# Optimization experiments

Hardware: AMD Instinct MI355X
Metric: run time of the kernel (lower is better)

Reference implementation:

```python
import jax, jax.numpy as jnp
import numpy as np

B, N, D_V, D_MODEL, D_FF, N_HEADS = 32, 64, 6, 128, 512, 8


def _ln(x, g, b):
    m = x.mean(-1, keepdims=True)
    v = ((x - m) ** 2).mean(-1, keepdims=True)
    return (x - m) / jnp.sqrt(v + 1e-5) * g + b


def _mha(q_in, k_in, v_in, mask, Wq, Wk, Wv, Wo):
    # mask: (b, Lq, Lk) bool, True = attend
    b, Lq, D = q_in.shape
    H, dh = N_HEADS, D_MODEL // N_HEADS
    q = (q_in @ Wq).reshape(b, Lq, H, dh)
    k = (k_in @ Wk).reshape(b, k_in.shape[1], H, dh)
    v = (v_in @ Wv).reshape(b, v_in.shape[1], H, dh)
    s = jnp.einsum('bqhd,bkhd->bhqk', q, k) / (dh ** 0.5)
    s = jnp.where(mask[:, None, :, :], s, -1e9)
    o = jnp.einsum('bhqk,bkhd->bqhd', jax.nn.softmax(s, axis=-1), v).reshape(b, Lq, D)
    return o @ Wo


def setup_inputs() -> dict:
    key = jax.random.key(0)
    ks = jax.random.split(key, 40)
    def p(i, shape, scale=0.05):
        return jax.random.normal(ks[i], shape, dtype=jnp.float32) * scale
    nm = jax.random.randint(ks[1], (B, N, N), 0, 2, dtype=jnp.int32)
    nm = nm.at[:, jnp.arange(N), jnp.arange(N)].set(1)  # self always a neighbor
    inp = {
        'agent_infos': jax.random.normal(ks[0], (B, N, N, D_V), dtype=jnp.float32),
        'neighbor_masks': nm,
        'padding_mask': jnp.ones((B, N), dtype=jnp.int32),
        'is_from_my_env': jnp.ones((B,), dtype=jnp.int32),
        # src_embed
        'W_emb': p(2, (D_V, D_MODEL)), 'b_emb': jnp.zeros((D_MODEL,), jnp.float32),
        # encoder layer (self-attn + FFN, post-LN)
        'Wq': p(3, (D_MODEL, D_MODEL)), 'Wk': p(4, (D_MODEL, D_MODEL)),
        'Wv': p(5, (D_MODEL, D_MODEL)), 'Wo': p(6, (D_MODEL, D_MODEL)),
        'ln1_g': jnp.ones((D_MODEL,), jnp.float32), 'ln1_b': jnp.zeros((D_MODEL,), jnp.float32),
        'W1': p(7, (D_MODEL, D_FF)), 'b1': jnp.zeros((D_FF,), jnp.float32),
        'W2': p(8, (D_FF, D_MODEL)), 'b2': jnp.zeros((D_MODEL,), jnp.float32),
        'ln2_g': jnp.ones((D_MODEL,), jnp.float32), 'ln2_b': jnp.zeros((D_MODEL,), jnp.float32),
        # decoder layer (cross-attn + FFN, post-LN)
        'Uq': p(9, (D_MODEL, D_MODEL)), 'Uk': p(10, (D_MODEL, D_MODEL)),
        'Uv': p(11, (D_MODEL, D_MODEL)), 'Uo': p(12, (D_MODEL, D_MODEL)),
        'ln3_g': jnp.ones((D_MODEL,), jnp.float32), 'ln3_b': jnp.zeros((D_MODEL,), jnp.float32),
        'W3': p(13, (D_MODEL, D_FF)), 'b3': jnp.zeros((D_FF,), jnp.float32),
        'W4': p(14, (D_FF, D_MODEL)), 'b4': jnp.zeros((D_MODEL,), jnp.float32),
        'ln4_g': jnp.ones((D_MODEL,), jnp.float32), 'ln4_b': jnp.zeros((D_MODEL,), jnp.float32),
        # generator (single-head query/key scorer)
        'Wg_q': p(15, (D_MODEL, D_MODEL)), 'Wg_k': p(16, (D_MODEL, D_MODEL)),
    }
    return inp


def reference(agent_infos, neighbor_masks, padding_mask, is_from_my_env,
              W_emb, b_emb, Wq, Wk, Wv, Wo, ln1_g, ln1_b, W1, b1, W2, b2, ln2_g, ln2_b,
              Uq, Uk, Uv, Uo, ln3_g, ln3_b, W3, b3, W4, b4, ln4_g, ln4_b, Wg_q, Wg_k):
    # Fold the per-agent python loop of the original into the batch dim: BN = B * N.
    src = agent_infos.reshape(B * N, N, D_V)
    neigh = neighbor_masks.reshape(B * N, N) != 0           # True = neighbor (attendable)
    x = src @ W_emb + b_emb                                 # (BN, N, D)
    src_mask = neigh[:, :, None] & neigh[:, None, :]        # (BN, N, N)
    x = _ln(x + _mha(x, x, x, src_mask, Wq, Wk, Wv, Wo), ln1_g, ln1_b)
    x = _ln(x + (jax.nn.relu(x @ W1 + b1) @ W2 + b2), ln2_g, ln2_b)
    # context vector -- faithful to the original get_context_vector (which sums rows
    # where pad_tokens==True, i.e. NON-neighbors, and divides by the neighbor count)
    pad = (~neigh)[:, :, None].astype(x.dtype)
    cnt = neigh.sum(axis=1).reshape(-1, 1, 1).astype(x.dtype)
    h_c = (x * pad).sum(axis=1, keepdims=True) / cnt        # (BN, 1, D)
    stm = neigh[:, None, :]                                 # src_tgt_mask (BN, 1, N)
    y = _ln(h_c + _mha(h_c, x, x, stm, Uq, Uk, Uv, Uo), ln3_g, ln3_b)
    y = _ln(y + (jax.nn.relu(y @ W3 + b3) @ W4 + b4), ln4_g, ln4_b)
    logits = jnp.einsum('bqd,bkd->bqk', y @ Wg_q, x @ Wg_k) / (D_MODEL ** 0.5)
    probs = jnp.where(stm, jax.nn.sigmoid(logits), 0.0)[:, 0, :]   # (BN, N)
    att_scores = probs.reshape(B, N, N)
    num_agents = padding_mask.sum(axis=1).astype(x.dtype).reshape(B, 1, 1)
    avg_h_c_N = h_c.reshape(B, N, D_MODEL).sum(axis=1, keepdims=True) / num_agents
    return att_scores, avg_h_c_N
```

## Files before the change

### kernel.cpp

```cpp
#include <hip/hip_runtime.h>
#include <hip/hip_bf16.h>
#include <math.h>

#define ITEMS 2048
#define SEQ   64
#define DM    128
#define DFF   512
#define ATT_OFF 131072

typedef unsigned short u16;
typedef __attribute__((ext_vector_type(4))) unsigned short ushort4v;
typedef __attribute__((ext_vector_type(8))) short short8v;
typedef __attribute__((ext_vector_type(4))) float float4v;

#define MFMA16(a,b,c) __builtin_amdgcn_mfma_f32_16x16x32_bf16(a,b,c,0,0,0)

#define XST 136
#define VST 72
#define PST 76

#define XS_B   0
#define QS_B   17408
#define KS_B   34816
#define VT_B   52224
#define PL_B   70656
#define ZB_B   80384
#define PF_B   80400
#define CNT_B  80656
#define NA_B   80660
#define NB_B   80664
#define ARENA_SZ 80672

#define HC_B   (KS_B+0)
#define QV_B   (KS_B+512)
#define OV_B   (KS_B+1024)
#define YV_B   (KS_B+1536)
#define Y2_B   (KS_B+2048)
#define GW_B   (KS_B+2560)
#define WALL_B (VT_B+0)
#define SALL_B (VT_B+4096)
#define PALL_B (VT_B+6144)
#define TALL_B (VT_B+8192)
#define FF_B   (VT_B+12288)
#define W4P_B  (VT_B+14336)

#define WQ_O   0
#define WK_O   16384
#define WV_O   32768
#define WO_O   49152
#define UK_O   65536
#define UV_O   81920
#define W1_O   98304
#define W2_O   163840
#define UQ_O   229376
#define UO_O   245760
#define WGQ_O  262144
#define WGK_O  278528
#define W3_O   294912
#define W4_O   360448
#define WS_TOT 425984

__device__ __forceinline__ u16 f2b(float f){
  union { float f; unsigned u; } v; v.f = f;
  unsigned r = (v.u + 0x7fffu + ((v.u >> 16) & 1u)) >> 16;
  return (u16)r;
}
__device__ __forceinline__ float b2f(u16 h){
  union { unsigned u; float f; } v; v.u = ((unsigned)h) << 16;
  return v.f;
}
__device__ __forceinline__ float wsum(float v){
  #pragma unroll
  for (int off = 1; off < 64; off <<= 1) v += __shfl_xor(v, off);
  return v;
}
__device__ __forceinline__ void ln_vec(float* v, const float* g, const float* b, int lane){
  float v0 = v[lane], v1 = v[lane+64];
  float m  = wsum(v0+v1) * (1.f/128.f);
  float d0 = v0-m, d1 = v1-m;
  float var = wsum(d0*d0+d1*d1) * (1.f/128.f);
  float inv = rsqrtf(var + 1e-5f);
  v[lane]    = d0*inv*g[lane]    + b[lane];
  v[lane+64] = d1*inv*g[lane+64] + b[lane+64];
}
__device__ __forceinline__ float dot128(const u16* __restrict__ wrow, const float* __restrict__ x){
  const short8v* wr = (const short8v*)wrow;
  float a = 0.f;
  #pragma unroll
  for (int c8 = 0; c8 < 16; c8++){
    short8v v = wr[c8];
    #pragma unroll
    for (int q = 0; q < 8; q++) a += b2f((u16)v[q]) * x[c8*8+q];
  }
  return a;
}

__global__ void prep_all(const float* __restrict__ Wq, const float* __restrict__ Wk,
                         const float* __restrict__ Wv, const float* __restrict__ Wo,
                         const float* __restrict__ Uk, const float* __restrict__ Uv,
                         const float* __restrict__ W1, const float* __restrict__ W2,
                         const float* __restrict__ Uq, const float* __restrict__ Uo,
                         const float* __restrict__ Wgq, const float* __restrict__ Wgk,
                         const float* __restrict__ W3, const float* __restrict__ W4,
                         u16* __restrict__ wts){
  int idx = blockIdx.x*256 + threadIdx.x;
  if (idx >= WS_TOT) return;
  float v;
  if (idx < 98304){
    int wsel = idx >> 14, r = idx & 16383;
    const float* tab[6] = {Wq,Wk,Wv,Wo,Uk,Uv};
    int o = r >> 7, i = r & 127;
    v = tab[wsel][i*128 + o];
  } else if (idx < W2_O){
    int r = idx - W1_O; int o = r >> 7, i = r & 127;
    v = W1[i*512 + o];
  } else if (idx < UQ_O){
    int r = idx - W2_O; int o = r >> 9, i = r & 511;
    v = W2[i*128 + o];
  } else if (idx < UO_O){
    int r = idx - UQ_O; int o = r >> 7, i = r & 127;
    v = Uq[i*128 + o];
  } else if (idx < WGQ_O){
    int r = idx - UO_O; int o = r >> 7, i = r & 127;
    v = Uo[i*128 + o];
  } else if (idx < WGK_O){
    int r = idx - WGQ_O; int o = r >> 7, i = r & 127;
    v = Wgq[i*128 + o];
  } else if (idx < W3_O){
    v = Wgk[idx - WGK_O];
  } else if (idx < W4_O){
    int r = idx - W3_O; int j = r >> 7, e = r & 127;
    v = W3[e*512 + j];
  } else {
    int r = idx - W4_O; int o = r >> 9, j = r & 511;
    v = W4[j*128 + o];
  }
  wts[idx] = f2b(v);
}

__global__ void init_avg(float* __restrict__ out){
  out[ATT_OFF + blockIdx.x*256 + threadIdx.x] = 0.f;
}

__global__ __launch_bounds__(256, 2) void vicsek_fused(
    const float* __restrict__ agent_infos,
    const int*   __restrict__ nmask,
    const int*   __restrict__ pmask,
    const u16*   __restrict__ wts,
    const float* __restrict__ W_emb, const float* __restrict__ b_emb,
    const float* __restrict__ ln1g,  const float* __restrict__ ln1b,
    const float* __restrict__ b1,    const float* __restrict__ b2,
    const float* __restrict__ ln2g,  const float* __restrict__ ln2b,
    const float* __restrict__ ln3g,  const float* __restrict__ ln3b,
    const float* __restrict__ b3,    const float* __restrict__ b4,
    const float* __restrict__ ln4g,  const float* __restrict__ ln4b,
    float* __restrict__ out)
{
  __shared__ __align__(16) char arena[ARENA_SZ];
  u16* Xs = (u16*)(arena + XS_B);
  u16* Qs = (u16*)(arena + QS_B);
  u16* Ks = (u16*)(arena + KS_B);
  u16* VT = (u16*)(arena + VT_B);
  u16* Pl = (u16*)(arena + PL_B);
  u16* zb = (u16*)(arena + ZB_B);
  float* padf  = (float*)(arena + PF_B);
  float* cnt_s = (float*)(arena + CNT_B);
  float* na_s  = (float*)(arena + NA_B);
  unsigned long long* nb_s = (unsigned long long*)(arena + NB_B);

  const int item = blockIdx.x;
  const int tid  = threadIdx.x;
  const int lane = tid & 63;
  const int w    = tid >> 6;
  const int row0 = w*16;
  const int arow = lane & 15;
  const int akg  = lane >> 4;

  const u16* WqT = wts + WQ_O;  const u16* WkT = wts + WK_O;
  const u16* WvT = wts + WV_O;  const u16* WoT = wts + WO_O;
  const u16* UkT = wts + UK_O;  const u16* UvT = wts + UV_O;
  const u16* W1T = wts + W1_O;  const u16* W2T = wts + W2_O;
  const u16* UqT = wts + UQ_O;  const u16* UoT = wts + UO_O;
  const u16* WgqT = wts + WGQ_O; const u16* WgkB = wts + WGK_O;
  const u16* W3T = wts + W3_O;  const u16* W4T = wts + W4_O;

  if (w == 0){
    int m = nmask[item*SEQ + lane];
    padf[lane] = m ? 0.f : 1.f;
    float c = wsum(m ? 1.f : 0.f);
    unsigned long long bb = __ballot(m != 0);
    if (lane == 0){ cnt_s[0] = c; nb_s[0] = bb; }
  }
  if (w == 1){
    float na = wsum((float)pmask[(item>>6)*SEQ + lane]);
    if (lane == 0) na_s[0] = na;
  }
  if (tid < 8) zb[tid] = 0;

  const float* src = agent_infos + (size_t)item*SEQ*6;
  for (int e = tid; e < SEQ*DM; e += 256){
    int r = e >> 7, c = e & 127;
    float a = b_emb[c];
    #pragma unroll
    for (int k = 0; k < 6; k++) a += src[r*6+k]*W_emb[k*DM+c];
    Xs[r*XST + c] = f2b(a);
  }
  __syncthreads();

  const unsigned long long nbits = nb_s[0];

  short8v aX[4];
  #pragma unroll
  for (int k = 0; k < 4; k++) aX[k] = *(const short8v*)(Xs + (row0+arow)*XST + k*32 + akg*8);

  for (int t = 0; t < 8; t++){
    const u16* wq = WqT + (t*16+arow)*128 + akg*8;
    const u16* wk = WkT + (t*16+arow)*128 + akg*8;
    const u16* wv = WvT + (t*16+arow)*128 + akg*8;
    float4v cq = {0,0,0,0}, ck = {0,0,0,0}, cv = {0,0,0,0};
    #pragma unroll
    for (int k = 0; k < 4; k++){
      cq = MFMA16(aX[k], *(const short8v*)(wq + k*32), cq);
      ck = MFMA16(aX[k], *(const short8v*)(wk + k*32), ck);
      cv = MFMA16(*(const short8v*)(wv + k*32), aX[k], cv);
    }
    #pragma unroll
    for (int i = 0; i < 4; i++){
      Qs[(row0+akg*4+i)*XST + t*16+arow] = f2b(cq[i]);
      Ks[(row0+akg*4+i)*XST + t*16+arow] = f2b(ck[i]);
      VT[(t*16+akg*4+i)*VST + row0+arow] = f2b(cv[i]);
    }
  }
  float4v accW[8];
  #pragma unroll
  for (int t = 0; t < 8; t++)
    #pragma unroll
    for (int i = 0; i < 4; i++)
      accW[t][i] = b2f(Xs[(row0+akg*4+i)*XST + t*16 + arow]);
  __syncthreads();

  for (int h = 0; h < 8; h++){
    const u16* qp = (akg < 2) ? (Qs + (row0+arow)*XST + h*16 + akg*8) : zb;
    short8v bq = *(const short8v*)qp;
    float4v st[4];
    #pragma unroll
    for (int kb = 0; kb < 4; kb++){
      const u16* kp = (akg < 2) ? (Ks + (kb*16+arow)*XST + h*16 + akg*8) : zb;
      float4v z = {0,0,0,0};
      st[kb] = MFMA16(*(const short8v*)kp, bq, z);
    }
    bool qok = (nbits >> (row0+arow)) & 1ull;
    float pr[16]; float mx = -3.0e38f;
    #pragma unroll
    for (int kb = 0; kb < 4; kb++)
      #pragma unroll
      for (int i = 0; i < 4; i++){
        int key = kb*16 + akg*4 + i;
        float s = st[kb][i]*0.25f;
        if (!qok || !((nbits>>key)&1ull)) s = -1.0e9f;
        pr[kb*4+i] = s; mx = fmaxf(mx, s);
      }
    mx = fmaxf(mx, __shfl_xor(mx,16)); mx = fmaxf(mx, __shfl_xor(mx,32));
    float sum = 0.f;
    #pragma unroll
    for (int z = 0; z < 16; z++){ pr[z] = __expf(pr[z]-mx); sum += pr[z]; }
    sum += __shfl_xor(sum,16); sum += __shfl_xor(sum,32);
    float inv = 1.f/sum;
    #pragma unroll
    for (int kb = 0; kb < 4; kb++)
      #pragma unroll
      for (int i = 0; i < 4; i++)
        Pl[(kb*16+akg*4+i)*PST + row0+arow] = f2b(pr[kb*4+i]*inv);
    float4v ot = {0,0,0,0};
    #pragma unroll
    for (int c2 = 0; c2 < 2; c2++){
      short8v av = *(const short8v*)(VT + (h*16+arow)*VST + c2*32 + akg*8);
      short8v bp;
      #pragma unroll
      for (int j = 0; j < 8; j++) bp[j] = (short)Pl[(c2*32+akg*8+j)*PST + row0+arow];
      ot = MFMA16(av, bp, ot);
    }
    ushort4v ov4;
    #pragma unroll
    for (int i = 0; i < 4; i++) ov4[i] = f2b(ot[i]);
    *(ushort4v*)(Xs + (row0+arow)*XST + h*16 + akg*4) = ov4;
  }

  {
    short8v aO[4];
    #pragma unroll
    for (int k = 0; k < 4; k++) aO[k] = *(const short8v*)(Xs + (row0+arow)*XST + k*32 + akg*8);
    #pragma unroll
    for (int k = 0; k < 4; k++)
      #pragma unroll
      for (int t = 0; t < 8; t++)
        accW[t] = MFMA16(aO[k], *(const short8v*)(WoT + (t*16+arow)*128 + k*32 + akg*8), accW[t]);
    float g8[8], bb8[8];
    #pragma unroll
    for (int t = 0; t < 8; t++){ g8[t] = ln1g[t*16+arow]; bb8[t] = ln1b[t*16+arow]; }
    #pragma unroll
    for (int i = 0; i < 4; i++){
      float sm = 0.f;
      #pragma unroll
      for (int t = 0; t < 8; t++) sm += accW[t][i];
      sm += __shfl_xor(sm,1); sm += __shfl_xor(sm,2); sm += __shfl_xor(sm,4); sm += __shfl_xor(sm,8);
      float mean = sm*(1.f/128.f);
      float vs = 0.f;
      #pragma unroll
      for (int t = 0; t < 8; t++){ float d = accW[t][i]-mean; vs += d*d; }
      vs += __shfl_xor(vs,1); vs += __shfl_xor(vs,2); vs += __shfl_xor(vs,4); vs += __shfl_xor(vs,8);
      float inv = rsqrtf(vs*(1.f/128.f) + 1e-5f);
      #pragma unroll
      for (int t = 0; t < 8; t++)
        Xs[(row0+akg*4+i)*XST + t*16 + arow] = f2b((accW[t][i]-mean)*inv*g8[t] + bb8[t]);
    }
  }
  #pragma unroll
  for (int k = 0; k < 4; k++) aX[k] = *(const short8v*)(Xs + (row0+arow)*XST + k*32 + akg*8);

  {
    u16* Hb = Qs;
    float4v accY[8];
    #pragma unroll
    for (int t = 0; t < 8; t++){
      float bb = b2[t*16 + arow];
      #pragma unroll
      for (int i = 0; i < 4; i++)
        accY[t][i] = bb + b2f(Xs[(row0+akg*4+i)*XST + t*16 + arow]);
    }
    for (int c = 0; c < 4; c++){
      #pragma unroll
      for (int t = 0; t < 8; t++){
        float bb = b1[c*128 + t*16 + arow];
        float4v acc = {bb,bb,bb,bb};
        #pragma unroll
        for (int k = 0; k < 4; k++)
          acc = MFMA16(aX[k], *(const short8v*)(W1T + (c*128+t*16+arow)*128 + k*32 + akg*8), acc);
        #pragma unroll
        for (int i = 0; i < 4; i++)
          Hb[(row0+akg*4+i)*XST + t*16 + arow] = f2b(fmaxf(acc[i], 0.f));
      }
      #pragma unroll
      for (int k = 0; k < 4; k++){
        short8v aH = *(const short8v*)(Hb + (row0+arow)*XST + k*32 + akg*8);
        #pragma unroll
        for (int t = 0; t < 8; t++)
          accY[t] = MFMA16(aH, *(const short8v*)(W2T + (t*16+arow)*512 + c*128 + k*32 + akg*8), accY[t]);
      }
    }
    float g8[8], bb8[8];
    #pragma unroll
    for (int t = 0; t < 8; t++){ g8[t] = ln2g[t*16+arow]; bb8[t] = ln2b[t*16+arow]; }
    #pragma unroll
    for (int i = 0; i < 4; i++){
      float sm = 0.f;
      #pragma unroll
      for (int t = 0; t < 8; t++) sm += accY[t][i];
      sm += __shfl_xor(sm,1); sm += __shfl_xor(sm,2); sm += __shfl_xor(sm,4); sm += __shfl_xor(sm,8);
      float mean = sm*(1.f/128.f);
      float vs = 0.f;
      #pragma unroll
      for (int t = 0; t < 8; t++){ float d = accY[t][i]-mean; vs += d*d; }
      vs += __shfl_xor(vs,1); vs += __shfl_xor(vs,2); vs += __shfl_xor(vs,4); vs += __shfl_xor(vs,8);
      float inv = rsqrtf(vs*(1.f/128.f) + 1e-5f);
      #pragma unroll
      for (int t = 0; t < 8; t++)
        Xs[(row0+akg*4+i)*XST + t*16 + arow] = f2b((accY[t][i]-mean)*inv*g8[t] + bb8[t]);
    }
  }
  __syncthreads();

  float* hc   = (float*)(arena + HC_B);
  float* qv   = (float*)(arena + QV_B);
  float* ov   = (float*)(arena + OV_B);
  float* yv   = (float*)(arena + YV_B);
  float* y2   = (float*)(arena + Y2_B);
  float* gw   = (float*)(arena + GW_B);
  float* wall = (float*)(arena + WALL_B);
  float* sall = (float*)(arena + SALL_B);
  float* pall = (float*)(arena + PALL_B);
  float* tall = (float*)(arena + TALL_B);
  float* ff   = (float*)(arena + FF_B);
  float* w4p  = (float*)(arena + W4P_B);

  if (tid < DM){
    float a = 0.f;
    #pragma unroll 8
    for (int r = 0; r < SEQ; r++) a += b2f(Xs[r*XST + tid]) * padf[r];
    a /= cnt_s[0];
    hc[tid] = a;
    atomicAdd(&out[ATT_OFF + (item>>6)*DM + tid], a/na_s[0]);
  }
  __syncthreads();

  if (tid < DM) qv[tid] = dot128(UqT + tid*128, hc);
  __syncthreads();
  if (tid < DM){
    #pragma unroll
    for (int h = 0; h < 8; h++){
      float a = 0.f;
      #pragma unroll
      for (int d = 0; d < 16; d++) a += b2f(UkT[(h*16+d)*128 + tid]) * qv[h*16+d];
      wall[h*128 + tid] = a;
    }
  }
  __syncthreads();
  for (int idx = tid; idx < 512; idx += 256){
    int h = idx >> 6, j = idx & 63;
    const short8v* xr = (const short8v*)(Xs + j*XST);
    const float* wv_ = wall + h*128;
    float a = 0.f;
    #pragma unroll
    for (int c8 = 0; c8 < 16; c8++){
      short8v v = xr[c8];
      #pragma unroll
      for (int q = 0; q < 8; q++) a += b2f((u16)v[q]) * wv_[c8*8+q];
    }
    sall[idx] = a*0.25f;
  }
  __syncthreads();
  for (int hh = w; hh < 8; hh += 4){
    float s = sall[hh*64 + lane];
    if (!((nbits>>lane)&1ull)) s = -1.0e9f;
    float mxx = s;
    #pragma unroll
    for (int off = 1; off < 64; off <<= 1) mxx = fmaxf(mxx, __shfl_xor(mxx, off));
    float p = __expf(s - mxx);
    float su = wsum(p);
    pall[hh*64 + lane] = p/su;
  }
  __syncthreads();
  {
    int task = tid >> 1, jh = tid & 1;
    int h = task >> 4, c8 = task & 15;
    float acc8[8] = {0,0,0,0,0,0,0,0};
    #pragma unroll 4
    for (int jj = 0; jj < 32; jj++){
      int j = jh*32 + jj;
      short8v v = *(const short8v*)(Xs + j*XST + c8*8);
      float pj = pall[h*64 + j];
      #pragma unroll
      for (int q = 0; q < 8; q++) acc8[q] += pj * b2f((u16)v[q]);
    }
    #pragma unroll
    for (int q = 0; q < 8; q++) acc8[q] += __shfl_xor(acc8[q], 1);
    if (jh == 0){
      #pragma unroll
      for (int q = 0; q < 8; q++) tall[h*128 + c8*8 + q] = acc8[q];
    }
  }
  __syncthreads();
  if (tid < DM) ov[tid] = dot128(UvT + tid*128, tall + (tid>>4)*128);
  __syncthreads();
  if (tid < DM) yv[tid] = hc[tid] + dot128(UoT + tid*128, ov);
  __syncthreads();
  if (w == 0) ln_vec(yv, ln3g, ln3b, lane);
  __syncthreads();

  for (int j = tid; j < DFF; j += 256)
    ff[j] = fmaxf(b3[j] + dot128(W3T + j*128, yv), 0.f);
  __syncthreads();
  {
    int o = tid & 127, half = tid >> 7;
    const short8v* wr = (const short8v*)(W4T + o*512 + half*256);
    const float* fh = ff + half*256;
    float a = 0.f;
    #pragma unroll
    for (int c8 = 0; c8 < 32; c8++){
      short8v v = wr[c8];
      #pragma unroll
      for (int q = 0; q < 8; q++) a += b2f((u16)v[q]) * fh[c8*8+q];
    }
    w4p[tid] = a;
  }
  __syncthreads();
  if (tid < DM) y2[tid] = b4[tid] + yv[tid] + w4p[tid] + w4p[tid+128];
  __syncthreads();
  if (w == 0) ln_vec(y2, ln4g, ln4b, lane);
  __syncthreads();

  if (tid < DM) qv[tid] = dot128(WgqT + tid*128, y2);
  __syncthreads();
  if (tid < DM) gw[tid] = dot128(WgkB + tid*128, qv);
  __syncthreads();
  if (tid < SEQ){
    float a = dot128(Xs + tid*XST, gw) ;
    a *= 0.08838834764831845f;
    out[(size_t)item*SEQ + tid] = ((nbits>>tid)&1ull) ? (1.f/(1.f+__expf(-a))) : 0.f;
  }
}

extern "C" void kernel_launch(void* const* d_in, const int* in_sizes, int n_in,
                              void* d_out, int out_size, void* d_ws, size_t ws_size,
                              hipStream_t stream)
{
  const float* agent_infos = (const float*)d_in[0];
  const int*   nmask       = (const int*)  d_in[1];
  const int*   pmask       = (const int*)  d_in[2];
  const float* W_emb = (const float*)d_in[4];
  const float* b_emb = (const float*)d_in[5];
  const float* Wq    = (const float*)d_in[6];
  const float* Wk    = (const float*)d_in[7];
  const float* Wv    = (const float*)d_in[8];
  const float* Wo    = (const float*)d_in[9];
  const float* ln1g  = (const float*)d_in[10];
  const float* ln1b  = (const float*)d_in[11];
  const float* W1    = (const float*)d_in[12];
  const float* b1    = (const float*)d_in[13];
  const float* W2    = (const float*)d_in[14];
  const float* b2    = (const float*)d_in[15];
  const float* ln2g  = (const float*)d_in[16];
  const float* ln2b  = (const float*)d_in[17];
  const float* Uq    = (const float*)d_in[18];
  const float* Uk    = (const float*)d_in[19];
  const float* Uv    = (const float*)d_in[20];
  const float* Uo    = (const float*)d_in[21];
  const float* ln3g  = (const float*)d_in[22];
  const float* ln3b  = (const float*)d_in[23];
  const float* W3    = (const float*)d_in[24];
  const float* b3    = (const float*)d_in[25];
  const float* W4    = (const float*)d_in[26];
  const float* b4    = (const float*)d_in[27];
  const float* ln4g  = (const float*)d_in[28];
  const float* ln4b  = (const float*)d_in[29];
  const float* Wgq   = (const float*)d_in[30];
  const float* Wgk   = (const float*)d_in[31];

  float* out = (float*)d_out;
  u16*   wts = (u16*)d_ws;

  prep_all<<<(WS_TOT+255)/256, 256, 0, stream>>>(Wq, Wk, Wv, Wo, Uk, Uv, W1, W2,
                                                 Uq, Uo, Wgq, Wgk, W3, W4, wts);
  init_avg<<<16, 256, 0, stream>>>(out);
  vicsek_fused<<<ITEMS, 256, 0, stream>>>(
      agent_infos, nmask, pmask, wts, W_emb, b_emb,
      ln1g, ln1b, b1, b2, ln2g, ln2b, ln3g, ln3b,
      b3, b4, ln4g, ln4b, out);
}
```

Measured before the change: 636.1 us.

## Process each item with a single wavefront and shrink shared memory

The fused kernel drops from 256 threads (4 waves) per item to one 64-lane wave that handles all four row groups. QKV projection now runs per head into small per-head buffers, and the LDS arena shrinks from about 80 KB to about 31 KB. All __syncthreads barriers go away, which should allow many more resident blocks per CU. The decoder cross-attention score and weighted-sum steps now use MFMA instead of scalar loops. In exchange, each wave does four times the work serially and holds a large register footprint (aX for all row groups plus packed residuals), which may cause spills or limit occupancy.

```diff
diff --git a/kernel.cpp b/kernel.cpp
--- a/kernel.cpp
+++ b/kernel.cpp
@@ -9,40 +9,38 @@
 #define ATT_OFF 131072
 
 typedef unsigned short u16;
+typedef unsigned int u32;
 typedef __attribute__((ext_vector_type(4))) unsigned short ushort4v;
 typedef __attribute__((ext_vector_type(8))) short short8v;
 typedef __attribute__((ext_vector_type(4))) float float4v;
 
 #define MFMA16(a,b,c) __builtin_amdgcn_mfma_f32_16x16x32_bf16(a,b,c,0,0,0)
 
-#define XST 136
-#define VST 72
-#define PST 76
+#define XST  136
+#define QST1 24
+#define VST1 72
+#define PST  20
 
 #define XS_B   0
-#define QS_B   17408
-#define KS_B   34816
-#define VT_B   52224
-#define PL_B   70656
-#define ZB_B   80384
-#define PF_B   80400
-#define CNT_B  80656
-#define NA_B   80660
-#define NB_B   80664
-#define ARENA_SZ 80672
-
-#define HC_B   (KS_B+0)
-#define QV_B   (KS_B+512)
-#define OV_B   (KS_B+1024)
-#define YV_B   (KS_B+1536)
-#define Y2_B   (KS_B+2048)
-#define GW_B   (KS_B+2560)
-#define WALL_B (VT_B+0)
-#define SALL_B (VT_B+4096)
-#define PALL_B (VT_B+6144)
-#define TALL_B (VT_B+8192)
-#define FF_B   (VT_B+12288)
-#define W4P_B  (VT_B+14336)
+#define Q1_B   17408
+#define K1_B   20480
+#define V1_B   23552
+#define PL_B   25856
+#define HC_B   28416
+#define QV_B   28928
+#define OV_B   29440
+#define YV_B   29952
+#define Y2_B   30464
+#define GW_B   30976
+#define ZB_B   31488
+#define ARENA_SZ 31504
+
+#define HBF_B   17408
+#define WALLB_B 17408
+#define SALL_B  19456
+#define PALL_B  21504
+#define TALL_B  17408
+#define FF_B    23552
 
 #define WQ_O   0
 #define WK_O   16384
@@ -142,7 +140,7 @@
   out[ATT_OFF + blockIdx.x*256 + threadIdx.x] = 0.f;
 }
 
-__global__ __launch_bounds__(256, 2) void vicsek_fused(
+__global__ __launch_bounds__(64, 2) void vicsek_fused(
     const float* __restrict__ agent_infos,
     const int*   __restrict__ nmask,
     const int*   __restrict__ pmask,
@@ -157,22 +155,15 @@
     float* __restrict__ out)
 {
   __shared__ __align__(16) char arena[ARENA_SZ];
-  u16* Xs = (u16*)(arena + XS_B);
-  u16* Qs = (u16*)(arena + QS_B);
-  u16* Ks = (u16*)(arena + KS_B);
-  u16* VT = (u16*)(arena + VT_B);
-  u16* Pl = (u16*)(arena + PL_B);
-  u16* zb = (u16*)(arena + ZB_B);
-  float* padf  = (float*)(arena + PF_B);
-  float* cnt_s = (float*)(arena + CNT_B);
-  float* na_s  = (float*)(arena + NA_B);
-  unsigned long long* nb_s = (unsigned long long*)(arena + NB_B);
+  u16* Xs  = (u16*)(arena + XS_B);
+  u16* Q1  = (u16*)(arena + Q1_B);
+  u16* K1  = (u16*)(arena + K1_B);
+  u16* V1T = (u16*)(arena + V1_B);
+  u16* Pl  = (u16*)(arena + PL_B);
+  u16* zb  = (u16*)(arena + ZB_B);
 
   const int item = blockIdx.x;
-  const int tid  = threadIdx.x;
-  const int lane = tid & 63;
-  const int w    = tid >> 6;
-  const int row0 = w*16;
+  const int lane = threadIdx.x;
   const int arow = lane & 15;
   const int akg  = lane >> 4;
 
@@ -184,309 +175,351 @@
   const u16* WgqT = wts + WGQ_O; const u16* WgkB = wts + WGK_O;
   const u16* W3T = wts + W3_O;  const u16* W4T = wts + W4_O;
 
-  if (w == 0){
-    int m = nmask[item*SEQ + lane];
-    padf[lane] = m ? 0.f : 1.f;
-    float c = wsum(m ? 1.f : 0.f);
-    unsigned long long bb = __ballot(m != 0);
-    if (lane == 0){ cnt_s[0] = c; nb_s[0] = bb; }
-  }
-  if (w == 1){
-    float na = wsum((float)pmask[(item>>6)*SEQ + lane]);
-    if (lane == 0) na_s[0] = na;
-  }
-  if (tid < 8) zb[tid] = 0;
-
-  const float* src = agent_infos + (size_t)item*SEQ*6;
-  for (int e = tid; e < SEQ*DM; e += 256){
-    int r = e >> 7, c = e & 127;
-    float a = b_emb[c];
-    #pragma unroll
-    for (int k = 0; k < 6; k++) a += src[r*6+k]*W_emb[k*DM+c];
-    Xs[r*XST + c] = f2b(a);
-  }
-  __syncthreads();
-
-  const unsigned long long nbits = nb_s[0];
-
-  short8v aX[4];
-  #pragma unroll
-  for (int k = 0; k < 4; k++) aX[k] = *(const short8v*)(Xs + (row0+arow)*XST + k*32 + akg*8);
-
-  for (int t = 0; t < 8; t++){
-    const u16* wq = WqT + (t*16+arow)*128 + akg*8;
-    const u16* wk = WkT + (t*16+arow)*128 + akg*8;
-    const u16* wv = WvT + (t*16+arow)*128 + akg*8;
-    float4v cq = {0,0,0,0}, ck = {0,0,0,0}, cv = {0,0,0,0};
-    #pragma unroll
-    for (int k = 0; k < 4; k++){
-      cq = MFMA16(aX[k], *(const short8v*)(wq + k*32), cq);
-      ck = MFMA16(aX[k], *(const short8v*)(wk + k*32), ck);
-      cv = MFMA16(*(const short8v*)(wv + k*32), aX[k], cv);
-    }
-    #pragma unroll
-    for (int i = 0; i < 4; i++){
-      Qs[(row0+akg*4+i)*XST + t*16+arow] = f2b(cq[i]);
-      Ks[(row0+akg*4+i)*XST + t*16+arow] = f2b(ck[i]);
-      VT[(t*16+akg*4+i)*VST + row0+arow] = f2b(cv[i]);
-    }
-  }
-  float4v accW[8];
-  #pragma unroll
-  for (int t = 0; t < 8; t++)
-    #pragma unroll
-    for (int i = 0; i < 4; i++)
-      accW[t][i] = b2f(Xs[(row0+akg*4+i)*XST + t*16 + arow]);
-  __syncthreads();
-
+  if (lane < 8) zb[lane] = 0;
+
+  int mm = nmask[item*SEQ + lane];
+  const unsigned long long nbits = __ballot(mm != 0);
+  const float cnt = (float)__popcll(nbits);
+  unsigned long long pb = __ballot(pmask[(item>>6)*SEQ + lane] != 0);
+  const float na = (float)__popcll(pb);
+
+  {
+    const float* src = agent_infos + (size_t)item*SEQ*6;
+    float we0[6], we1[6];
+    #pragma unroll
+    for (int k = 0; k < 6; k++){ we0[k] = W_emb[k*DM+lane]; we1[k] = W_emb[k*DM+lane+64]; }
+    float be0 = b_emb[lane], be1 = b_emb[lane+64];
+    for (int r = 0; r < SEQ; r++){
+      float a0 = be0, a1 = be1;
+      #pragma unroll
+      for (int k = 0; k < 6; k++){ float s = src[r*6+k]; a0 += s*we0[k]; a1 += s*we1[k]; }
+      Xs[r*XST + lane]    = f2b(a0);
+      Xs[r*XST + lane+64] = f2b(a1);
+    }
+  }
+
+  short8v aX[4][4];
+  #pragma unroll
+  for (int rg = 0; rg < 4; rg++)
+    #pragma unroll
+    for (int k = 0; k < 4; k++)
+      aX[rg][k] = *(const short8v*)(Xs + (rg*16+arow)*XST + k*32 + akg*8);
+  u32 resid[4][8][2];
+  #pragma unroll
+  for (int rg = 0; rg < 4; rg++)
+    #pragma unroll
+    for (int t = 0; t < 8; t++){
+      u16 x0 = Xs[(rg*16+akg*4+0)*XST + t*16+arow];
+      u16 x1 = Xs[(rg*16+akg*4+1)*XST + t*16+arow];
+      u16 x2 = Xs[(rg*16+akg*4+2)*XST + t*16+arow];
+      u16 x3 = Xs[(rg*16+akg*4+3)*XST + t*16+arow];
+      resid[rg][t][0] = (u32)x0 | ((u32)x1 << 16);
+      resid[rg][t][1] = (u32)x2 | ((u32)x3 << 16);
+    }
+
+  #pragma unroll 1
   for (int h = 0; h < 8; h++){
-    const u16* qp = (akg < 2) ? (Qs + (row0+arow)*XST + h*16 + akg*8) : zb;
-    short8v bq = *(const short8v*)qp;
-    float4v st[4];
-    #pragma unroll
-    for (int kb = 0; kb < 4; kb++){
-      const u16* kp = (akg < 2) ? (Ks + (kb*16+arow)*XST + h*16 + akg*8) : zb;
-      float4v z = {0,0,0,0};
-      st[kb] = MFMA16(*(const short8v*)kp, bq, z);
-    }
-    bool qok = (nbits >> (row0+arow)) & 1ull;
-    float pr[16]; float mx = -3.0e38f;
-    #pragma unroll
-    for (int kb = 0; kb < 4; kb++)
+    {
+      short8v bw[4];
+      #pragma unroll
+      for (int k = 0; k < 4; k++) bw[k] = *(const short8v*)(WqT + (h*16+arow)*128 + k*32 + akg*8);
+      #pragma unroll
+      for (int rg = 0; rg < 4; rg++){
+        float4v c = {0,0,0,0};
+        #pragma unroll
+        for (int k = 0; k < 4; k++) c = MFMA16(aX[rg][k], bw[k], c);
+        #pragma unroll
+        for (int i = 0; i < 4; i++) Q1[(rg*16+akg*4+i)*QST1 + arow] = f2b(c[i]);
+      }
+      #pragma unroll
+      for (int k = 0; k < 4; k++) bw[k] = *(const short8v*)(WkT + (h*16+arow)*128 + k*32 + akg*8);
+      #pragma unroll
+      for (int rg = 0; rg < 4; rg++){
+        float4v c = {0,0,0,0};
+        #pragma unroll
+        for (int k = 0; k < 4; k++) c = MFMA16(aX[rg][k], bw[k], c);
+        #pragma unroll
+        for (int i = 0; i < 4; i++) K1[(rg*16+akg*4+i)*QST1 + arow] = f2b(c[i]);
+      }
+      #pragma unroll
+      for (int k = 0; k < 4; k++) bw[k] = *(const short8v*)(WvT + (h*16+arow)*128 + k*32 + akg*8);
+      #pragma unroll
+      for (int rg = 0; rg < 4; rg++){
+        float4v c = {0,0,0,0};
+        #pragma unroll
+        for (int k = 0; k < 4; k++) c = MFMA16(bw[k], aX[rg][k], c);
+        #pragma unroll
+        for (int i = 0; i < 4; i++) V1T[(akg*4+i)*VST1 + rg*16+arow] = f2b(c[i]);
+      }
+    }
+    for (int qt = 0; qt < 4; qt++){
+      const u16* qp = (akg < 2) ? (Q1 + (qt*16+arow)*QST1 + akg*8) : zb;
+      short8v bq = *(const short8v*)qp;
+      float4v st[4];
+      #pragma unroll
+      for (int kb = 0; kb < 4; kb++){
+        const u16* kp = (akg < 2) ? (K1 + (kb*16+arow)*QST1 + akg*8) : zb;
+        float4v z = {0,0,0,0};
+        st[kb] = MFMA16(*(const short8v*)kp, bq, z);
+      }
+      bool qok = (nbits >> (qt*16+arow)) & 1ull;
+      float pr[16]; float mx = -3.0e38f;
+      #pragma unroll
+      for (int kb = 0; kb < 4; kb++)
+        #pragma unroll
+        for (int i = 0; i < 4; i++){
+          int key = kb*16 + akg*4 + i;
+          float s = st[kb][i]*0.25f;
+          if (!qok || !((nbits>>key)&1ull)) s = -1.0e9f;
+          pr[kb*4+i] = s; mx = fmaxf(mx, s);
+        }
+      mx = fmaxf(mx, __shfl_xor(mx,16)); mx = fmaxf(mx, __shfl_xor(mx,32));
+      float sum = 0.f;
+      #pragma unroll
+      for (int z2 = 0; z2 < 16; z2++){ pr[z2] = __expf(pr[z2]-mx); sum += pr[z2]; }
+      sum += __shfl_xor(sum,16); sum += __shfl_xor(sum,32);
+      float inv = 1.f/sum;
+      #pragma unroll
+      for (int kb = 0; kb < 4; kb++)
+        #pragma unroll
+        for (int i = 0; i < 4; i++)
+          Pl[(kb*16+akg*4+i)*PST + arow] = f2b(pr[kb*4+i]*inv);
+      float4v ot = {0,0,0,0};
+      #pragma unroll
+      for (int c2 = 0; c2 < 2; c2++){
+        short8v av = *(const short8v*)(V1T + arow*VST1 + c2*32 + akg*8);
+        short8v bp;
+        #pragma unroll
+        for (int j = 0; j < 8; j++) bp[j] = (short)Pl[(c2*32+akg*8+j)*PST + arow];
+        ot = MFMA16(av, bp, ot);
+      }
+      ushort4v ov4;
+      #pragma unroll
+      for (int i = 0; i < 4; i++) ov4[i] = f2b(ot[i]);
+      *(ushort4v*)(Xs + (qt*16+arow)*XST + h*16 + akg*4) = ov4;
+    }
+  }
+
+  {
+    float g8[8], bb8[8];
+    #pragma unroll
+    for (int t = 0; t < 8; t++){ g8[t] = ln1g[t*16+arow]; bb8[t] = ln1b[t*16+arow]; }
+    #pragma unroll
+    for (int rg = 0; rg < 4; rg++){
+      float4v acc[8];
+      #pragma unroll
+      for (int t = 0; t < 8; t++){
+        acc[t][0] = b2f((u16)(resid[rg][t][0] & 0xffff));
+        acc[t][1] = b2f((u16)(resid[rg][t][0] >> 16));
+        acc[t][2] = b2f((u16)(resid[rg][t][1] & 0xffff));
+        acc[t][3] = b2f((u16)(resid[rg][t][1] >> 16));
+      }
+      short8v aO[4];
+      #pragma unroll
+      for (int k = 0; k < 4; k++) aO[k] = *(const short8v*)(Xs + (rg*16+arow)*XST + k*32 + akg*8);
+      #pragma unroll
+      for (int k = 0; k < 4; k++)
+        #pragma unroll
+        for (int t = 0; t < 8; t++)
+          acc[t] = MFMA16(aO[k], *(const short8v*)(WoT + (t*16+arow)*128 + k*32 + akg*8), acc[t]);
       #pragma unroll
       for (int i = 0; i < 4; i++){
-        int key = kb*16 + akg*4 + i;
-        float s = st[kb][i]*0.25f;
-        if (!qok || !((nbits>>key)&1ull)) s = -1.0e9f;
-        pr[kb*4+i] = s; mx = fmaxf(mx, s);
-      }
-    mx = fmaxf(mx, __shfl_xor(mx,16)); mx = fmaxf(mx, __shfl_xor(mx,32));
-    float sum = 0.f;
-    #pragma unroll
-    for (int z = 0; z < 16; z++){ pr[z] = __expf(pr[z]-mx); sum += pr[z]; }
-    sum += __shfl_xor(sum,16); sum += __shfl_xor(sum,32);
-    float inv = 1.f/sum;
-    #pragma unroll
-    for (int kb = 0; kb < 4; kb++)
-      #pragma unroll
-      for (int i = 0; i < 4; i++)
-        Pl[(kb*16+akg*4+i)*PST + row0+arow] = f2b(pr[kb*4+i]*inv);
-    float4v ot = {0,0,0,0};
-    #pragma unroll
-    for (int c2 = 0; c2 < 2; c2++){
-      short8v av = *(const short8v*)(VT + (h*16+arow)*VST + c2*32 + akg*8);
-      short8v bp;
-      #pragma unroll
-      for (int j = 0; j < 8; j++) bp[j] = (short)Pl[(c2*32+akg*8+j)*PST + row0+arow];
-      ot = MFMA16(av, bp, ot);
-    }
-    ushort4v ov4;
-    #pragma unroll
-    for (int i = 0; i < 4; i++) ov4[i] = f2b(ot[i]);
-    *(ushort4v*)(Xs + (row0+arow)*XST + h*16 + akg*4) = ov4;
+        float sm = 0.f;
+        #pragma unroll
+        for (int t = 0; t < 8; t++) sm += acc[t][i];
+        sm += __shfl_xor(sm,1); sm += __shfl_xor(sm,2); sm += __shfl_xor(sm,4); sm += __shfl_xor(sm,8);
+        float mean = sm*(1.f/128.f);
+        float vs = 0.f;
+        #pragma unroll
+        for (int t = 0; t < 8; t++){ float d = acc[t][i]-mean; vs += d*d; }
+        vs += __shfl_xor(vs,1); vs += __shfl_xor(vs,2); vs += __shfl_xor(vs,4); vs += __shfl_xor(vs,8);
+        float inv = rsqrtf(vs*(1.f/128.f) + 1e-5f);
+        #pragma unroll
+        for (int t = 0; t < 8; t++)
+          Xs[(rg*16+akg*4+i)*XST + t*16 + arow] = f2b((acc[t][i]-mean)*inv*g8[t] + bb8[t]);
+      }
+    }
   }
 
   {
-    short8v aO[4];
-    #pragma unroll
-    for (int k = 0; k < 4; k++) aO[k] = *(const short8v*)(Xs + (row0+arow)*XST + k*32 + akg*8);
-    #pragma unroll
-    for (int k = 0; k < 4; k++)
-      #pragma unroll
-      for (int t = 0; t < 8; t++)
-        accW[t] = MFMA16(aO[k], *(const short8v*)(WoT + (t*16+arow)*128 + k*32 + akg*8), accW[t]);
+    u16* Hb = (u16*)(arena + HBF_B);
     float g8[8], bb8[8];
     #pragma unroll
-    for (int t = 0; t < 8; t++){ g8[t] = ln1g[t*16+arow]; bb8[t] = ln1b[t*16+arow]; }
-    #pragma unroll
-    for (int i = 0; i < 4; i++){
-      float sm = 0.f;
-      #pragma unroll
-      for (int t = 0; t < 8; t++) sm += accW[t][i];
-      sm += __shfl_xor(sm,1); sm += __shfl_xor(sm,2); sm += __shfl_xor(sm,4); sm += __shfl_xor(sm,8);
-      float mean = sm*(1.f/128.f);
-      float vs = 0.f;
-      #pragma unroll
-      for (int t = 0; t < 8; t++){ float d = accW[t][i]-mean; vs += d*d; }
-      vs += __shfl_xor(vs,1); vs += __shfl_xor(vs,2); vs += __shfl_xor(vs,4); vs += __shfl_xor(vs,8);
-      float inv = rsqrtf(vs*(1.f/128.f) + 1e-5f);
-      #pragma unroll
-      for (int t = 0; t < 8; t++)
-        Xs[(row0+akg*4+i)*XST + t*16 + arow] = f2b((accW[t][i]-mean)*inv*g8[t] + bb8[t]);
-    }
-  }
-  #pragma unroll
-  for (int k = 0; k < 4; k++) aX[k] = *(const short8v*)(Xs + (row0+arow)*XST + k*32 + akg*8);
+    for (int t = 0; t < 8; t++){ g8[t] = ln2g[t*16+arow]; bb8[t] = ln2b[t*16+arow]; }
+    #pragma unroll 1
+    for (int rg = 0; rg < 4; rg++){
+      float4v accY[8];
+      #pragma unroll
+      for (int t = 0; t < 8; t++){
+        float bb = b2[t*16 + arow];
+        #pragma unroll
+        for (int i = 0; i < 4; i++)
+          accY[t][i] = bb + b2f(Xs[(rg*16+akg*4+i)*XST + t*16 + arow]);
+      }
+      short8v aXf[4];
+      #pragma unroll
+      for (int k = 0; k < 4; k++) aXf[k] = *(const short8v*)(Xs + (rg*16+arow)*XST + k*32 + akg*8);
+      #pragma unroll 1
+      for (int c = 0; c < 4; c++){
+        #pragma unroll
+        for (int t = 0; t < 8; t++){
+          float bb = b1[c*128 + t*16 + arow];
+          float4v hid = {bb,bb,bb,bb};
+          #pragma unroll
+          for (int k = 0; k < 4; k++)
+            hid = MFMA16(aXf[k], *(const short8v*)(W1T + (c*128+t*16+arow)*128 + k*32 + akg*8), hid);
+          #pragma unroll
+          for (int i = 0; i < 4; i++)
+            Hb[(akg*4+i)*XST + t*16 + arow] = f2b(fmaxf(hid[i], 0.f));
+        }
+        #pragma unroll
+        for (int k = 0; k < 4; k++){
+          short8v aH = *(const short8v*)(Hb + arow*XST + k*32 + akg*8);
+          #pragma unroll
+          for (int t = 0; t < 8; t++)
+            accY[t] = MFMA16(aH, *(const short8v*)(W2T + (t*16+arow)*512 + c*128 + k*32 + akg*8), accY[t]);
+        }
+      }
+      #pragma unroll
+      for (int i = 0; i < 4; i++){
+        float sm = 0.f;
+        #pragma unroll
+        for (int t = 0; t < 8; t++) sm += accY[t][i];
+        sm += __shfl_xor(sm,1); sm += __shfl_xor(sm,2); sm += __shfl_xor(sm,4); sm += __shfl_xor(sm,8);
+        float mean = sm*(1.f/128.f);
+        float vs = 0.f;
+        #pragma unroll
+        for (int t = 0; t < 8; t++){ float d = accY[t][i]-mean; vs += d*d; }
+        vs += __shfl_xor(vs,1); vs += __shfl_xor(vs,2); vs += __shfl_xor(vs,4); vs += __shfl_xor(vs,8);
+        float inv = rsqrtf(vs*(1.f/128.f) + 1e-5f);
+        #pragma unroll
+        for (int t = 0; t < 8; t++)
+          Xs[(rg*16+akg*4+i)*XST + t*16 + arow] = f2b((accY[t][i]-mean)*inv*g8[t] + bb8[t]);
+      }
+    }
+  }
+
+  float* hc = (float*)(arena + HC_B);
+  float* qv = (float*)(arena + QV_B);
+  float* ov = (float*)(arena + OV_B);
+  float* yv = (float*)(arena + YV_B);
+  float* y2 = (float*)(arena + Y2_B);
+  float* gw = (float*)(arena + GW_B);
 
   {
-    u16* Hb = Qs;
-    float4v accY[8];
-    #pragma unroll
-    for (int t = 0; t < 8; t++){
-      float bb = b2[t*16 + arow];
-      #pragma unroll
-      for (int i = 0; i < 4; i++)
-        accY[t][i] = bb + b2f(Xs[(row0+akg*4+i)*XST + t*16 + arow]);
-    }
-    for (int c = 0; c < 4; c++){
-      #pragma unroll
-      for (int t = 0; t < 8; t++){
-        float bb = b1[c*128 + t*16 + arow];
-        float4v acc = {bb,bb,bb,bb};
-        #pragma unroll
-        for (int k = 0; k < 4; k++)
-          acc = MFMA16(aX[k], *(const short8v*)(W1T + (c*128+t*16+arow)*128 + k*32 + akg*8), acc);
-        #pragma unroll
-        for (int i = 0; i < 4; i++)
-          Hb[(row0+akg*4+i)*XST + t*16 + arow] = f2b(fmaxf(acc[i], 0.f));
-      }
-      #pragma unroll
-      for (int k = 0; k < 4; k++){
-        short8v aH = *(const short8v*)(Hb + (row0+arow)*XST + k*32 + akg*8);
-        #pragma unroll
-        for (int t = 0; t < 8; t++)
-          accY[t] = MFMA16(aH, *(const short8v*)(W2T + (t*16+arow)*512 + c*128 + k*32 + akg*8), accY[t]);
-      }
-    }
-    float g8[8], bb8[8];
-    #pragma unroll
-    for (int t = 0; t < 8; t++){ g8[t] = ln2g[t*16+arow]; bb8[t] = ln2b[t*16+arow]; }
-    #pragma unroll
-    for (int i = 0; i < 4; i++){
-      float sm = 0.f;
-      #pragma unroll
-      for (int t = 0; t < 8; t++) sm += accY[t][i];
-      sm += __shfl_xor(sm,1); sm += __shfl_xor(sm,2); sm += __shfl_xor(sm,4); sm += __shfl_xor(sm,8);
-      float mean = sm*(1.f/128.f);
-      float vs = 0.f;
-      #pragma unroll
-      for (int t = 0; t < 8; t++){ float d = accY[t][i]-mean; vs += d*d; }
-      vs += __shfl_xor(vs,1); vs += __shfl_xor(vs,2); vs += __shfl_xor(vs,4); vs += __shfl_xor(vs,8);
-      float inv = rsqrtf(vs*(1.f/128.f) + 1e-5f);
-      #pragma unroll
-      for (int t = 0; t < 8; t++)
-        Xs[(row0+akg*4+i)*XST + t*16 + arow] = f2b((accY[t][i]-mean)*inv*g8[t] + bb8[t]);
-    }
-  }
-  __syncthreads();
-
-  float* hc   = (float*)(arena + HC_B);
-  float* qv   = (float*)(arena + QV_B);
-  float* ov   = (float*)(arena + OV_B);
-  float* yv   = (float*)(arena + YV_B);
-  float* y2   = (float*)(arena + Y2_B);
-  float* gw   = (float*)(arena + GW_B);
-  float* wall = (float*)(arena + WALL_B);
-  float* sall = (float*)(arena + SALL_B);
-  float* pall = (float*)(arena + PALL_B);
-  float* tall = (float*)(arena + TALL_B);
-  float* ff   = (float*)(arena + FF_B);
-  float* w4p  = (float*)(arena + W4P_B);
-
-  if (tid < DM){
-    float a = 0.f;
-    #pragma unroll 8
-    for (int r = 0; r < SEQ; r++) a += b2f(Xs[r*XST + tid]) * padf[r];
-    a /= cnt_s[0];
-    hc[tid] = a;
-    atomicAdd(&out[ATT_OFF + (item>>6)*DM + tid], a/na_s[0]);
-  }
-  __syncthreads();
-
-  if (tid < DM) qv[tid] = dot128(UqT + tid*128, hc);
-  __syncthreads();
-  if (tid < DM){
+    float a0 = 0.f, a1 = 0.f;
+    for (int r = 0; r < SEQ; r++){
+      float pf = ((nbits>>r)&1ull) ? 0.f : 1.f;
+      a0 += b2f(Xs[r*XST + lane])    * pf;
+      a1 += b2f(Xs[r*XST + lane+64]) * pf;
+    }
+    a0 /= cnt; a1 /= cnt;
+    hc[lane] = a0; hc[lane+64] = a1;
+    atomicAdd(&out[ATT_OFF + (item>>6)*DM + lane],    a0/na);
+    atomicAdd(&out[ATT_OFF + (item>>6)*DM + lane+64], a1/na);
+  }
+
+  qv[lane]    = dot128(UqT + lane*128,      hc);
+  qv[lane+64] = dot128(UqT + (lane+64)*128, hc);
+
+  u16* wallb = (u16*)(arena + WALLB_B);
+  #pragma unroll
+  for (int half = 0; half < 2; half++){
+    int e2 = lane + half*64;
     #pragma unroll
     for (int h = 0; h < 8; h++){
       float a = 0.f;
       #pragma unroll
-      for (int d = 0; d < 16; d++) a += b2f(UkT[(h*16+d)*128 + tid]) * qv[h*16+d];
-      wall[h*128 + tid] = a;
-    }
-  }
-  __syncthreads();
-  for (int idx = tid; idx < 512; idx += 256){
-    int h = idx >> 6, j = idx & 63;
-    const short8v* xr = (const short8v*)(Xs + j*XST);
-    const float* wv_ = wall + h*128;
-    float a = 0.f;
-    #pragma unroll
-    for (int c8 = 0; c8 < 16; c8++){
-      short8v v = xr[c8];
-      #pragma unroll
-      for (int q = 0; q < 8; q++) a += b2f((u16)v[q]) * wv_[c8*8+q];
-    }
-    sall[idx] = a*0.25f;
-  }
-  __syncthreads();
-  for (int hh = w; hh < 8; hh += 4){
-    float s = sall[hh*64 + lane];
+      for (int d = 0; d < 16; d++) a += b2f(UkT[(h*16+d)*128 + e2]) * qv[h*16+d];
+      wallb[h*128 + e2] = f2b(a);
+    }
+  }
+
+  float* sall = (float*)(arena + SALL_B);
+  #pragma unroll
+  for (int rg = 0; rg < 4; rg++){
+    short8v aXf[4];
+    #pragma unroll
+    for (int k = 0; k < 4; k++) aXf[k] = *(const short8v*)(Xs + (rg*16+arow)*XST + k*32 + akg*8);
+    float4v sc = {0,0,0,0};
+    #pragma unroll
+    for (int k = 0; k < 4; k++){
+      short8v bw = *(const short8v*)(wallb + arow*128 + k*32 + akg*8);
+      sc = MFMA16(aXf[k], bw, sc);
+    }
+    if (arow < 8){
+      #pragma unroll
+      for (int i = 0; i < 4; i++) sall[arow*64 + rg*16 + akg*4 + i] = sc[i]*0.25f;
+    }
+  }
+
+  float* pall = (float*)(arena + PALL_B);
+  #pragma unroll 1
+  for (int h = 0; h < 8; h++){
+    float s = sall[h*64 + lane];
     if (!((nbits>>lane)&1ull)) s = -1.0e9f;
     float mxx = s;
     #pragma unroll
     for (int off = 1; off < 64; off <<= 1) mxx = fmaxf(mxx, __shfl_xor(mxx, off));
     float p = __expf(s - mxx);
     float su = wsum(p);
-    pall[hh*64 + lane] = p/su;
-  }
-  __syncthreads();
+    pall[h*64 + lane] = p/su;
+  }
+
+  float* tall = (float*)(arena + TALL_B);
+  #pragma unroll 1
+  for (int ct = 0; ct < 8; ct++){
+    float4v tc = {0,0,0,0};
+    #pragma unroll
+    for (int k2 = 0; k2 < 2; k2++){
+      short8v ap, bx;
+      #pragma unroll
+      for (int j = 0; j < 8; j++){
+        ap[j] = (short)f2b(pall[arow*64 + k2*32 + akg*8 + j]);
+        bx[j] = (short)Xs[(k2*32+akg*8+j)*XST + ct*16 + arow];
+      }
+      tc = MFMA16(ap, bx, tc);
+    }
+    if (akg < 2){
+      #pragma unroll
+      for (int i = 0; i < 4; i++) tall[(akg*4+i)*128 + ct*16 + arow] = tc[i];
+    }
+  }
+
+  ov[lane]    = dot128(UvT + lane*128,      tall + (lane>>4)*128);
+  ov[lane+64] = dot128(UvT + (lane+64)*128, tall + ((lane+64)>>4)*128);
+  yv[lane]    = hc[lane]    + dot128(UoT + lane*128,      ov);
+  yv[lane+64] = hc[lane+64] + dot128(UoT + (lane+64)*128, ov);
+  ln_vec(yv, ln3g, ln3b, lane);
+
+  float* ff = (float*)(arena + FF_B);
+  #pragma unroll 1
+  for (int jj = 0; jj < 8; jj++){
+    int j = jj*64 + lane;
+    ff[j] = fmaxf(b3[j] + dot128(W3T + j*128, yv), 0.f);
+  }
+  #pragma unroll
+  for (int half = 0; half < 2; half++){
+    int e2 = lane + half*64;
+    const short8v* wr = (const short8v*)(W4T + e2*512);
+    float a = 0.f;
+    #pragma unroll
+    for (int c8 = 0; c8 < 64; c8++){
+      short8v v = wr[c8];
+      #pragma unroll
+      for (int q = 0; q < 8; q++) a += b2f((u16)v[q]) * ff[c8*8+q];
+    }
+    y2[e2] = b4[e2] + yv[e2] + a;
+  }
+  ln_vec(y2, ln4g, ln4b, lane);
+
+  qv[lane]    = dot128(WgqT + lane*128,      y2);
+  qv[lane+64] = dot128(WgqT + (lane+64)*128, y2);
+  gw[lane]    = dot128(WgkB + lane*128,      qv);
+  gw[lane+64] = dot128(WgkB + (lane+64)*128, qv);
   {
-    int task = tid >> 1, jh = tid & 1;
-    int h = task >> 4, c8 = task & 15;
-    float acc8[8] = {0,0,0,0,0,0,0,0};
-    #pragma unroll 4
-    for (int jj = 0; jj < 32; jj++){
-      int j = jh*32 + jj;
-      short8v v = *(const short8v*)(Xs + j*XST + c8*8);
-      float pj = pall[h*64 + j];
-      #pragma unroll
-      for (int q = 0; q < 8; q++) acc8[q] += pj * b2f((u16)v[q]);
-    }
-    #pragma unroll
-    for (int q = 0; q < 8; q++) acc8[q] += __shfl_xor(acc8[q], 1);
-    if (jh == 0){
-      #pragma unroll
-      for (int q = 0; q < 8; q++) tall[h*128 + c8*8 + q] = acc8[q];
-    }
-  }
-  __syncthreads();
-  if (tid < DM) ov[tid] = dot128(UvT + tid*128, tall + (tid>>4)*128);
-  __syncthreads();
-  if (tid < DM) yv[tid] = hc[tid] + dot128(UoT + tid*128, ov);
-  __syncthreads();
-  if (w == 0) ln_vec(yv, ln3g, ln3b, lane);
-  __syncthreads();
-
-  for (int j = tid; j < DFF; j += 256)
-    ff[j] = fmaxf(b3[j] + dot128(W3T + j*128, yv), 0.f);
-  __syncthreads();
-  {
-    int o = tid & 127, half = tid >> 7;
-    const short8v* wr = (const short8v*)(W4T + o*512 + half*256);
-    const float* fh = ff + half*256;
-    float a = 0.f;
-    #pragma unroll
-    for (int c8 = 0; c8 < 32; c8++){
-      short8v v = wr[c8];
-      #pragma unroll
-      for (int q = 0; q < 8; q++) a += b2f((u16)v[q]) * fh[c8*8+q];
-    }
-    w4p[tid] = a;
-  }
-  __syncthreads();
-  if (tid < DM) y2[tid] = b4[tid] + yv[tid] + w4p[tid] + w4p[tid+128];
-  __syncthreads();
-  if (w == 0) ln_vec(y2, ln4g, ln4b, lane);
-  __syncthreads();
-
-  if (tid < DM) qv[tid] = dot128(WgqT + tid*128, y2);
-  __syncthreads();
-  if (tid < DM) gw[tid] = dot128(WgkB + tid*128, qv);
-  __syncthreads();
-  if (tid < SEQ){
-    float a = dot128(Xs + tid*XST, gw) ;
-    a *= 0.08838834764831845f;
-    out[(size_t)item*SEQ + tid] = ((nbits>>tid)&1ull) ? (1.f/(1.f+__expf(-a))) : 0.f;
+    float a = dot128(Xs + lane*XST, gw) * 0.08838834764831845f;
+    out[(size_t)item*SEQ + lane] = ((nbits>>lane)&1ull) ? (1.f/(1.f+__expf(-a))) : 0.f;
   }
 }
 
@@ -532,7 +565,7 @@
   prep_all<<<(WS_TOT+255)/256, 256, 0, stream>>>(Wq, Wk, Wv, Wo, Uk, Uv, W1, W2,
                                                  Uq, Uo, Wgq, Wgk, W3, W4, wts);
   init_avg<<<16, 256, 0, stream>>>(out);
-  vicsek_fused<<<ITEMS, 256, 0, stream>>>(
+  vicsek_fused<<<ITEMS, 64, 0, stream>>>(
       agent_infos, nmask, pmask, wts, W_emb, b_emb,
       ln1g, ln1b, b1, b2, ln2g, ln2b, ln3g, ln3b,
       b3, b4, ln4g, ln4b, out);
```

Result: slower. 956.3 us (+50.4%).
